# Kernel optimization log

Hardware: AMD Instinct MI355X
Metric: run time of the kernel (lower is better)

Reference implementation:

```python
import jax, jax.numpy as jnp
import numpy as np

LEVELS = 25  # constructor default, used in forward


def setup_inputs() -> dict:
    key = jax.random.key(0)
    ks = jax.random.split(key, 7)
    B, D_in, H, D_out = 131072, 512, 512, 128
    s_in = 1.0 / np.sqrt(D_in)
    s_h = 1.0 / np.sqrt(H)
    return {
        "x": jax.random.normal(ks[0], (B, D_in), jnp.float32),
        "W_in": jax.random.uniform(ks[1], (D_in, H), jnp.float32, -s_in, s_in),
        "b_in": jax.random.uniform(ks[2], (H,), jnp.float32, -s_in, s_in),
        "W_h": jax.random.uniform(ks[3], (H, H), jnp.float32, -s_h, s_h),
        "b_h": jax.random.uniform(ks[4], (H,), jnp.float32, -s_h, s_h),
        "W_out": jax.random.uniform(ks[5], (H, D_out), jnp.float32, -s_h, s_h),
        "b_out": jax.random.uniform(ks[6], (D_out,), jnp.float32, -s_h, s_h),
    }


def _discretize(x, levels):
    # Equal-width bins per column: np.linspace(min, max, levels+1)[1:-1]
    # -> levels-1 interior boundaries: min + (max-min)*k/levels, k=1..levels-1
    b_min = x.min(axis=0)  # [D]
    b_max = x.max(axis=0)  # [D]
    frac = jnp.arange(1, levels, dtype=x.dtype) / levels  # [levels-1]
    bounds = b_min[:, None] + (b_max - b_min)[:, None] * frac[None, :]  # [D, levels-1]
    # torch.bucketize(right=False) == searchsorted side='left', per column
    idx = jax.vmap(
        lambda col, b: jnp.searchsorted(b, col, side="left"),
        in_axes=(1, 0), out_axes=1,
    )(x, bounds)  # [B, D] int32
    # torch.tensor(X_discre, dtype=float32) detaches from the graph
    return jax.lax.stop_gradient(idx.astype(jnp.float32))


def reference(x, W_in, b_in, W_h, b_h, W_out, b_out):
    d = _discretize(x, LEVELS)                 # [B, D_in]
    h = jax.nn.relu(d @ W_in + b_in)           # l_in
    for _ in range(5):
        h = jax.nn.relu(h @ W_h + b_h)
    y = jax.nn.relu(h @ W_out + b_out)         # l_out
    d2_loss = jnp.zeros((), jnp.float32)
    return (y, d2_loss)
```

## Files before the change

### kernel.cpp

```cpp
#include <hip/hip_runtime.h>
#include <hip/hip_bf16.h>

typedef unsigned short u16;
typedef unsigned int u32;
typedef __attribute__((ext_vector_type(8))) short s16x8;
typedef __attribute__((ext_vector_type(4))) float f32x4;

__device__ __forceinline__ u16 bf16bits(float v) {
    union { __hip_bfloat16 b; u16 u; } c;
    c.b = __float2bfloat16(v);
    return c.u;
}

__device__ __forceinline__ float disc1(float v, float mn, float rg, float s) {
    const float u = __fmul_rn(__fsub_rn(v, mn), s);
    const float rn = rintf(u);
    int idx;
    if (fabsf(u - rn) > 1e-3f) {
        idx = (int)ceilf(u) - 1;
    } else {
        int kc = (int)rn;
        kc = kc < 1 ? 1 : (kc > 24 ? 24 : kc);
        const float cf = __fdiv_rn((float)kc, 25.0f);
        const float b = __fadd_rn(mn, __fmul_rn(rg, cf));
        idx = (int)rn - 1 + ((b < v) ? 1 : 0);
    }
    idx = idx < 0 ? 0 : (idx > 24 ? 24 : idx);
    return (float)idx;
}

__global__ void kminmax(const float* __restrict__ x, float* __restrict__ pmin,
                        float* __restrict__ pmax) {
    __shared__ float4 smn[512], smx[512];
    const int t = threadIdx.x;
    const int c4 = t & 127;
    const int ro = t >> 7;
    const size_t r0 = (size_t)blockIdx.x * 128;
    float4 mn = {1e30f, 1e30f, 1e30f, 1e30f};
    float4 mx = {-1e30f, -1e30f, -1e30f, -1e30f};
#pragma unroll 8
    for (int i = 0; i < 32; ++i) {
        const int row = ro + i * 4;
        const float4 v = ((const float4*)(x + (r0 + row) * 512))[c4];
        mn.x = fminf(mn.x, v.x); mn.y = fminf(mn.y, v.y);
        mn.z = fminf(mn.z, v.z); mn.w = fminf(mn.w, v.w);
        mx.x = fmaxf(mx.x, v.x); mx.y = fmaxf(mx.y, v.y);
        mx.z = fmaxf(mx.z, v.z); mx.w = fmaxf(mx.w, v.w);
    }
    smn[t] = mn; smx[t] = mx;
    __syncthreads();
    if (t < 128) {
#pragma unroll
        for (int p = 1; p < 4; ++p) {
            const float4 a = smn[t + p * 128], b = smx[t + p * 128];
            mn.x = fminf(mn.x, a.x); mn.y = fminf(mn.y, a.y);
            mn.z = fminf(mn.z, a.z); mn.w = fminf(mn.w, a.w);
            mx.x = fmaxf(mx.x, b.x); mx.y = fmaxf(mx.y, b.y);
            mx.z = fmaxf(mx.z, b.z); mx.w = fmaxf(mx.w, b.w);
        }
        ((float4*)(pmin + blockIdx.x * 512))[c4] = mn;
        ((float4*)(pmax + blockIdx.x * 512))[c4] = mx;
    }
}

__global__ void kred(const float* __restrict__ pmin, const float* __restrict__ pmax,
                     float* __restrict__ p2min, float* __restrict__ p2max, int per) {
    const int c = threadIdx.x;
    const int j = blockIdx.x;
    float mn = 1e30f, mx = -1e30f;
    for (int i = 0; i < per; ++i) {
        mn = fminf(mn, pmin[(size_t)(j * per + i) * 512 + c]);
        mx = fmaxf(mx, pmax[(size_t)(j * per + i) * 512 + c]);
    }
    p2min[j * 512 + c] = mn;
    p2max[j * 512 + c] = mx;
}

__global__ void kbounds(const float* __restrict__ p2min, const float* __restrict__ p2max,
                        float* __restrict__ cmin, float* __restrict__ crange,
                        float* __restrict__ sinv, int np, float* __restrict__ dloss) {
    const int c = threadIdx.x;
    float mn = 1e30f, mx = -1e30f;
    for (int p = 0; p < np; ++p) {
        mn = fminf(mn, p2min[p * 512 + c]);
        mx = fmaxf(mx, p2max[p * 512 + c]);
    }
    cmin[c] = mn;
    const float rg = __fsub_rn(mx, mn);
    crange[c] = rg;
    sinv[c] = __fdiv_rn(25.0f, rg);
    if (c == 0) dloss[0] = 0.0f;
}

__global__ void ktc_all(const float* __restrict__ W_in, const float* __restrict__ W_h,
                        const float* __restrict__ W_out,
                        __hip_bfloat16* __restrict__ WinT, __hip_bfloat16* __restrict__ WhT,
                        __hip_bfloat16* __restrict__ WoutT) {
    const int i = blockIdx.x * 256 + threadIdx.x;
    if (i < 512 * 512) {
        WinT[i] = __float2bfloat16(W_in[(size_t)(i & 511) * 512 + (i >> 9)]);
    } else if (i < 2 * 512 * 512) {
        const int j = i - 512 * 512;
        WhT[j] = __float2bfloat16(W_h[(size_t)(j & 511) * 512 + (j >> 9)]);
    } else if (i < 2 * 512 * 512 + 128 * 512) {
        const int j = i - 2 * 512 * 512;
        WoutT[j] = __float2bfloat16(W_out[(size_t)(j & 511) * 128 + (j >> 9)]);
    }
}

__global__ __launch_bounds__(512, 2) void megamlp(
    const float* __restrict__ x,
    const float* __restrict__ cmin, const float* __restrict__ crange,
    const float* __restrict__ sinv,
    const u16* __restrict__ WinT, const u16* __restrict__ WhT,
    const u16* __restrict__ WoutT,
    const float* __restrict__ b_in, const float* __restrict__ b_h,
    const float* __restrict__ b_out,
    float* __restrict__ out) {
    __shared__ __attribute__((aligned(16))) u16 actA[64 * 512];
    __shared__ __attribute__((aligned(16))) u16 actB[64 * 512];

    const int t = threadIdx.x;
    const int lane = t & 63;
    const int w = t >> 6;
    const int lr = lane & 15;
    const int kq = lane >> 4;
    const int xr = lr & 7;
    const size_t row0 = (size_t)blockIdx.x * 128;

    {
        const int c4 = t & 127;
        const int ro = t >> 7;
        const float4 mn4 = ((const float4*)cmin)[c4];
        const float4 rg4 = ((const float4*)crange)[c4];
        const float4 s4  = ((const float4*)sinv)[c4];
        const int g16 = c4 >> 1;
        const int hb  = (c4 & 1) << 3;
#pragma unroll 8
        for (int i = 0; i < 32; ++i) {
            const int row = ro + i * 4;
            const float4 v = ((const float4*)(x + (row0 + row) * 512))[c4];
            const u32 lo = (u32)bf16bits(disc1(v.x, mn4.x, rg4.x, s4.x))
                         | ((u32)bf16bits(disc1(v.y, mn4.y, rg4.y, s4.y)) << 16);
            const u32 hi = (u32)bf16bits(disc1(v.z, mn4.z, rg4.z, s4.z))
                         | ((u32)bf16bits(disc1(v.w, mn4.w, rg4.w, s4.w)) << 16);
            const int rl = row & 63;
            const int gg = g16 ^ (rl & 7);
            char* base = (row < 64) ? (char*)actA : (char*)actB;
            *(uint2*)(base + (rl << 10) + (gg << 4) + hb) = make_uint2(lo, hi);
        }
    }
    __syncthreads();

    for (int layer = 0; layer < 6; ++layer) {
        const u16* W = (layer == 0) ? WinT : WhT;
        const float* bias = (layer == 0) ? b_in : b_h;

        f32x4 acc[2][4][4] = {};
        const u16* wp0 = W + ((w * 64 + lr) << 9) + (kq << 3);

        s16x8 aF[4], aN[4];
#pragma unroll
        for (int mt = 0; mt < 4; ++mt)
            aF[mt] = *(const s16x8*)(wp0 + (mt << 13));

#pragma unroll
        for (int ks = 0; ks < 16; ++ks) {
            if (ks < 15) {
                const u16* wn = wp0 + (ks + 1) * 32;
#pragma unroll
                for (int mt = 0; mt < 4; ++mt)
                    aN[mt] = *(const s16x8*)(wn + (mt << 13));
            }
            const int gg = ((ks << 2) | kq) ^ xr;
#pragma unroll
            for (int h = 0; h < 2; ++h) {
                const char* ah = h ? (const char*)actB : (const char*)actA;
                s16x8 bF[4];
#pragma unroll
                for (int nt = 0; nt < 4; ++nt)
                    bF[nt] = *(const s16x8*)(ah + ((nt * 16 + lr) << 10) + (gg << 4));
#pragma unroll
                for (int mt = 0; mt < 4; ++mt)
#pragma unroll
                    for (int nt = 0; nt < 4; ++nt)
                        acc[h][mt][nt] = __builtin_amdgcn_mfma_f32_16x16x32_bf16(
                            aF[mt], bF[nt], acc[h][mt][nt], 0, 0, 0);
            }
#pragma unroll
            for (int mt = 0; mt < 4; ++mt) aF[mt] = aN[mt];
        }
        __syncthreads();

#pragma unroll
        for (int mt = 0; mt < 4; ++mt) {
            const int g16 = w * 8 + mt * 2 + (kq >> 1);
            float bv[4];
#pragma unroll
            for (int r = 0; r < 4; ++r)
                bv[r] = bias[w * 64 + mt * 16 + kq * 4 + r];
#pragma unroll
            for (int h = 0; h < 2; ++h) {
                char* ah = h ? (char*)actB : (char*)actA;
#pragma unroll
                for (int nt = 0; nt < 4; ++nt) {
                    const int batch = nt * 16 + lr;
                    const float v0 = fmaxf(acc[h][mt][nt][0] + bv[0], 0.0f);
                    const float v1 = fmaxf(acc[h][mt][nt][1] + bv[1], 0.0f);
                    const float v2 = fmaxf(acc[h][mt][nt][2] + bv[2], 0.0f);
                    const float v3 = fmaxf(acc[h][mt][nt][3] + bv[3], 0.0f);
                    const u32 lo = (u32)bf16bits(v0) | ((u32)bf16bits(v1) << 16);
                    const u32 hi = (u32)bf16bits(v2) | ((u32)bf16bits(v3) << 16);
                    const int gg = g16 ^ (batch & 7);
                    *(uint2*)(ah + (batch << 10) + (gg << 4) + ((kq & 1) << 3)) =
                        make_uint2(lo, hi);
                }
            }
        }
        __syncthreads();
    }

    {
        f32x4 acc[2][4] = {};
        const u16* wp = WoutT + ((w * 16 + lr) << 9) + (kq << 3);
        s16x8 aF = *(const s16x8*)(wp);
#pragma unroll
        for (int ks = 0; ks < 16; ++ks) {
            s16x8 aN;
            if (ks < 15) aN = *(const s16x8*)(wp + (ks + 1) * 32);
            const int gg = ((ks << 2) | kq) ^ xr;
#pragma unroll
            for (int h = 0; h < 2; ++h) {
                const char* ah = h ? (const char*)actB : (const char*)actA;
#pragma unroll
                for (int nt = 0; nt < 4; ++nt) {
                    const s16x8 bF = *(const s16x8*)(ah + ((nt * 16 + lr) << 10) + (gg << 4));
                    acc[h][nt] = __builtin_amdgcn_mfma_f32_16x16x32_bf16(
                        aF, bF, acc[h][nt], 0, 0, 0);
                }
            }
            aF = aN;
        }
        __syncthreads();

        float bv[4];
#pragma unroll
        for (int r = 0; r < 4; ++r) bv[r] = b_out[w * 16 + kq * 4 + r];
        const int g16o = w * 4 + kq;
#pragma unroll
        for (int h = 0; h < 2; ++h) {
            char* sh = h ? (char*)actB : (char*)actA;
#pragma unroll
            for (int nt = 0; nt < 4; ++nt) {
                const int batch = nt * 16 + lr;
                const int gg = g16o ^ (batch & 7);
                float* p = (float*)(sh + (batch << 9) + (gg << 4));
#pragma unroll
                for (int r = 0; r < 4; ++r)
                    p[r] = fmaxf(acc[h][nt][r] + bv[r], 0.0f);
            }
        }
    }
    __syncthreads();

    {
        const int n4 = t & 31;
        const int bo = t >> 5;
#pragma unroll
        for (int h = 0; h < 2; ++h) {
            const char* sh = h ? (const char*)actB : (const char*)actA;
#pragma unroll
            for (int pp = 0; pp < 4; ++pp) {
                const int batch = pp * 16 + bo;
                const int gg = n4 ^ (batch & 7);
                const float4 v = *(const float4*)(sh + (batch << 9) + (gg << 4));
                ((float4*)(out + (row0 + h * 64 + batch) * 128))[n4] = v;
            }
        }
    }
}

extern "C" void kernel_launch(void* const* d_in, const int* in_sizes, int n_in,
                              void* d_out, int out_size, void* d_ws, size_t ws_size,
                              hipStream_t stream) {
    const float* x     = (const float*)d_in[0];
    const float* W_in  = (const float*)d_in[1];
    const float* b_in  = (const float*)d_in[2];
    const float* W_h   = (const float*)d_in[3];
    const float* b_h   = (const float*)d_in[4];
    const float* W_out = (const float*)d_in[5];
    const float* b_out = (const float*)d_in[6];
    float* out = (float*)d_out;

    const int B = in_sizes[0] / 512;
    const int NP1 = B / 128;

    __hip_bfloat16* WinT  = (__hip_bfloat16*)d_ws;
    __hip_bfloat16* WhT   = WinT + 512 * 512;
    __hip_bfloat16* WoutT = WhT + 512 * 512;
    float* pmin   = (float*)(WoutT + 128 * 512);
    float* pmax   = pmin + (size_t)NP1 * 512;
    float* p2min  = pmax + (size_t)NP1 * 512;
    float* p2max  = p2min + 64 * 512;
    float* cmin   = p2max + 64 * 512;
    float* crange = cmin + 512;
    float* sinv   = crange + 512;

    kminmax<<<NP1, 512, 0, stream>>>(x, pmin, pmax);
    kred<<<64, 512, 0, stream>>>(pmin, pmax, p2min, p2max, NP1 / 64);
    kbounds<<<1, 512, 0, stream>>>(p2min, p2max, cmin, crange, sinv, 64,
                                   out + (size_t)B * 128);
    ktc_all<<<(2 * 512 * 512 + 128 * 512 + 255) / 256, 256, 0, stream>>>(
        W_in, W_h, W_out, WinT, WhT, WoutT);

    megamlp<<<B / 128, 512, 0, stream>>>(x, cmin, crange, sinv,
        (const u16*)WinT, (const u16*)WhT, (const u16*)WoutT,
        b_in, b_h, b_out, out);
}
```

Baseline: 956.0 us.

## Halve rows per block in fused MLP to raise occupancy

Each block of the fused MLP kernel now processes 64 batch rows instead of 128, using a single 64 KB LDS activation buffer instead of two. Launch bounds are raised to 4 blocks per CU and the grid doubles. The register prefetch of weight fragments for the next k-step is dropped, and bias loads become vectorized. The aim is more resident waves to hide latency, at the cost of reading each weight fragment from global/L2 twice as often per row processed.

```diff
diff --git a/kernel.cpp b/kernel.cpp
--- a/kernel.cpp
+++ b/kernel.cpp
@@ -108,7 +108,7 @@
     }
 }
 
-__global__ __launch_bounds__(512, 2) void megamlp(
+__global__ __launch_bounds__(512, 4) void megamlp(
     const float* __restrict__ x,
     const float* __restrict__ cmin, const float* __restrict__ crange,
     const float* __restrict__ sinv,
@@ -117,8 +117,7 @@
     const float* __restrict__ b_in, const float* __restrict__ b_h,
     const float* __restrict__ b_out,
     float* __restrict__ out) {
-    __shared__ __attribute__((aligned(16))) u16 actA[64 * 512];
-    __shared__ __attribute__((aligned(16))) u16 actB[64 * 512];
+    __shared__ __attribute__((aligned(16))) u16 act[64 * 512];
 
     const int t = threadIdx.x;
     const int lane = t & 63;
@@ -126,7 +125,7 @@
     const int lr = lane & 15;
     const int kq = lane >> 4;
     const int xr = lr & 7;
-    const size_t row0 = (size_t)blockIdx.x * 128;
+    const size_t row0 = (size_t)blockIdx.x * 64;
 
     {
         const int c4 = t & 127;
@@ -136,18 +135,16 @@
         const float4 s4  = ((const float4*)sinv)[c4];
         const int g16 = c4 >> 1;
         const int hb  = (c4 & 1) << 3;
-#pragma unroll 8
-        for (int i = 0; i < 32; ++i) {
+#pragma unroll 4
+        for (int i = 0; i < 16; ++i) {
             const int row = ro + i * 4;
             const float4 v = ((const float4*)(x + (row0 + row) * 512))[c4];
             const u32 lo = (u32)bf16bits(disc1(v.x, mn4.x, rg4.x, s4.x))
                          | ((u32)bf16bits(disc1(v.y, mn4.y, rg4.y, s4.y)) << 16);
             const u32 hi = (u32)bf16bits(disc1(v.z, mn4.z, rg4.z, s4.z))
                          | ((u32)bf16bits(disc1(v.w, mn4.w, rg4.w, s4.w)) << 16);
-            const int rl = row & 63;
-            const int gg = g16 ^ (rl & 7);
-            char* base = (row < 64) ? (char*)actA : (char*)actB;
-            *(uint2*)(base + (rl << 10) + (gg << 4) + hb) = make_uint2(lo, hi);
+            const int gg = g16 ^ (row & 7);
+            *(uint2*)((char*)act + (row << 10) + (gg << 4) + hb) = make_uint2(lo, hi);
         }
     }
     __syncthreads();
@@ -156,109 +153,76 @@
         const u16* W = (layer == 0) ? WinT : WhT;
         const float* bias = (layer == 0) ? b_in : b_h;
 
-        f32x4 acc[2][4][4] = {};
+        f32x4 acc[4][4] = {};
         const u16* wp0 = W + ((w * 64 + lr) << 9) + (kq << 3);
 
-        s16x8 aF[4], aN[4];
-#pragma unroll
-        for (int mt = 0; mt < 4; ++mt)
-            aF[mt] = *(const s16x8*)(wp0 + (mt << 13));
-
 #pragma unroll
         for (int ks = 0; ks < 16; ++ks) {
-            if (ks < 15) {
-                const u16* wn = wp0 + (ks + 1) * 32;
-#pragma unroll
-                for (int mt = 0; mt < 4; ++mt)
-                    aN[mt] = *(const s16x8*)(wn + (mt << 13));
-            }
+            s16x8 aF[4], bF[4];
+            const u16* wp = wp0 + ks * 32;
+#pragma unroll
+            for (int mt = 0; mt < 4; ++mt)
+                aF[mt] = *(const s16x8*)(wp + (mt << 13));
             const int gg = ((ks << 2) | kq) ^ xr;
 #pragma unroll
-            for (int h = 0; h < 2; ++h) {
-                const char* ah = h ? (const char*)actB : (const char*)actA;
-                s16x8 bF[4];
+            for (int nt = 0; nt < 4; ++nt)
+                bF[nt] = *(const s16x8*)((const char*)act + ((nt * 16 + lr) << 10) + (gg << 4));
+#pragma unroll
+            for (int mt = 0; mt < 4; ++mt)
 #pragma unroll
                 for (int nt = 0; nt < 4; ++nt)
-                    bF[nt] = *(const s16x8*)(ah + ((nt * 16 + lr) << 10) + (gg << 4));
-#pragma unroll
-                for (int mt = 0; mt < 4; ++mt)
-#pragma unroll
-                    for (int nt = 0; nt < 4; ++nt)
-                        acc[h][mt][nt] = __builtin_amdgcn_mfma_f32_16x16x32_bf16(
-                            aF[mt], bF[nt], acc[h][mt][nt], 0, 0, 0);
-            }
-#pragma unroll
-            for (int mt = 0; mt < 4; ++mt) aF[mt] = aN[mt];
+                    acc[mt][nt] = __builtin_amdgcn_mfma_f32_16x16x32_bf16(
+                        aF[mt], bF[nt], acc[mt][nt], 0, 0, 0);
         }
         __syncthreads();
 
 #pragma unroll
         for (int mt = 0; mt < 4; ++mt) {
+            const f32x4 bv = ((const f32x4*)bias)[w * 16 + mt * 4 + kq];
             const int g16 = w * 8 + mt * 2 + (kq >> 1);
-            float bv[4];
-#pragma unroll
-            for (int r = 0; r < 4; ++r)
-                bv[r] = bias[w * 64 + mt * 16 + kq * 4 + r];
-#pragma unroll
-            for (int h = 0; h < 2; ++h) {
-                char* ah = h ? (char*)actB : (char*)actA;
-#pragma unroll
-                for (int nt = 0; nt < 4; ++nt) {
-                    const int batch = nt * 16 + lr;
-                    const float v0 = fmaxf(acc[h][mt][nt][0] + bv[0], 0.0f);
-                    const float v1 = fmaxf(acc[h][mt][nt][1] + bv[1], 0.0f);
-                    const float v2 = fmaxf(acc[h][mt][nt][2] + bv[2], 0.0f);
-                    const float v3 = fmaxf(acc[h][mt][nt][3] + bv[3], 0.0f);
-                    const u32 lo = (u32)bf16bits(v0) | ((u32)bf16bits(v1) << 16);
-                    const u32 hi = (u32)bf16bits(v2) | ((u32)bf16bits(v3) << 16);
-                    const int gg = g16 ^ (batch & 7);
-                    *(uint2*)(ah + (batch << 10) + (gg << 4) + ((kq & 1) << 3)) =
-                        make_uint2(lo, hi);
-                }
-            }
-        }
-        __syncthreads();
-    }
-
-    {
-        f32x4 acc[2][4] = {};
-        const u16* wp = WoutT + ((w * 16 + lr) << 9) + (kq << 3);
-        s16x8 aF = *(const s16x8*)(wp);
-#pragma unroll
-        for (int ks = 0; ks < 16; ++ks) {
-            s16x8 aN;
-            if (ks < 15) aN = *(const s16x8*)(wp + (ks + 1) * 32);
-            const int gg = ((ks << 2) | kq) ^ xr;
-#pragma unroll
-            for (int h = 0; h < 2; ++h) {
-                const char* ah = h ? (const char*)actB : (const char*)actA;
-#pragma unroll
-                for (int nt = 0; nt < 4; ++nt) {
-                    const s16x8 bF = *(const s16x8*)(ah + ((nt * 16 + lr) << 10) + (gg << 4));
-                    acc[h][nt] = __builtin_amdgcn_mfma_f32_16x16x32_bf16(
-                        aF, bF, acc[h][nt], 0, 0, 0);
-                }
-            }
-            aF = aN;
-        }
-        __syncthreads();
-
-        float bv[4];
-#pragma unroll
-        for (int r = 0; r < 4; ++r) bv[r] = b_out[w * 16 + kq * 4 + r];
-        const int g16o = w * 4 + kq;
-#pragma unroll
-        for (int h = 0; h < 2; ++h) {
-            char* sh = h ? (char*)actB : (char*)actA;
 #pragma unroll
             for (int nt = 0; nt < 4; ++nt) {
                 const int batch = nt * 16 + lr;
-                const int gg = g16o ^ (batch & 7);
-                float* p = (float*)(sh + (batch << 9) + (gg << 4));
-#pragma unroll
-                for (int r = 0; r < 4; ++r)
-                    p[r] = fmaxf(acc[h][nt][r] + bv[r], 0.0f);
+                const float v0 = fmaxf(acc[mt][nt][0] + bv[0], 0.0f);
+                const float v1 = fmaxf(acc[mt][nt][1] + bv[1], 0.0f);
+                const float v2 = fmaxf(acc[mt][nt][2] + bv[2], 0.0f);
+                const float v3 = fmaxf(acc[mt][nt][3] + bv[3], 0.0f);
+                const u32 lo = (u32)bf16bits(v0) | ((u32)bf16bits(v1) << 16);
+                const u32 hi = (u32)bf16bits(v2) | ((u32)bf16bits(v3) << 16);
+                const int gg = g16 ^ (batch & 7);
+                *(uint2*)((char*)act + (batch << 10) + (gg << 4) + ((kq & 1) << 3)) =
+                    make_uint2(lo, hi);
             }
+        }
+        __syncthreads();
+    }
+
+    {
+        f32x4 acc[4] = {};
+        const u16* wp = WoutT + ((w * 16 + lr) << 9) + (kq << 3);
+#pragma unroll
+        for (int ks = 0; ks < 16; ++ks) {
+            const s16x8 aF = *(const s16x8*)(wp + ks * 32);
+            const int gg = ((ks << 2) | kq) ^ xr;
+#pragma unroll
+            for (int nt = 0; nt < 4; ++nt) {
+                const s16x8 bF = *(const s16x8*)((const char*)act + ((nt * 16 + lr) << 10) + (gg << 4));
+                acc[nt] = __builtin_amdgcn_mfma_f32_16x16x32_bf16(
+                    aF, bF, acc[nt], 0, 0, 0);
+            }
+        }
+        __syncthreads();
+
+        const f32x4 bvo = ((const f32x4*)b_out)[w * 4 + kq];
+        const int g16o = w * 4 + kq;
+#pragma unroll
+        for (int nt = 0; nt < 4; ++nt) {
+            const int batch = nt * 16 + lr;
+            const int gg = g16o ^ (batch & 7);
+            float* p = (float*)((char*)act + (batch << 9) + (gg << 4));
+#pragma unroll
+            for (int r = 0; r < 4; ++r)
+                p[r] = fmaxf(acc[nt][r] + bvo[r], 0.0f);
         }
     }
     __syncthreads();
@@ -267,15 +231,11 @@
         const int n4 = t & 31;
         const int bo = t >> 5;
 #pragma unroll
-        for (int h = 0; h < 2; ++h) {
-            const char* sh = h ? (const char*)actB : (const char*)actA;
-#pragma unroll
-            for (int pp = 0; pp < 4; ++pp) {
-                const int batch = pp * 16 + bo;
-                const int gg = n4 ^ (batch & 7);
-                const float4 v = *(const float4*)(sh + (batch << 9) + (gg << 4));
-                ((float4*)(out + (row0 + h * 64 + batch) * 128))[n4] = v;
-            }
+        for (int pp = 0; pp < 4; ++pp) {
+            const int batch = pp * 16 + bo;
+            const int gg = n4 ^ (batch & 7);
+            const float4 v = *(const float4*)((const char*)act + (batch << 9) + (gg << 4));
+            ((float4*)(out + (row0 + batch) * 128))[n4] = v;
         }
     }
 }
@@ -313,7 +273,7 @@
     ktc_all<<<(2 * 512 * 512 + 128 * 512 + 255) / 256, 256, 0, stream>>>(
         W_in, W_h, W_out, WinT, WhT, WoutT);
 
-    megamlp<<<B / 128, 512, 0, stream>>>(x, cmin, crange, sinv,
+    megamlp<<<B / 64, 512, 0, stream>>>(x, cmin, crange, sinv,
         (const u16*)WinT, (const u16*)WhT, (const u16*)WoutT,
         b_in, b_h, b_out, out);
 }
```

Result: slower. 1.200 ms (+25.5%).

## Switch hidden layers to 32x32x16 MFMA tiles with setprio around MFMA bursts

Applied to the files above, without the earlier changes.

Replaces the 16x16x32 bf16 MFMA tiling in the six 512x512 layers with 32x32x16 MFMAs on 2x2 tiles per half-batch. This cuts the number of LDS fragment loads per MFMA and the instruction count. It also drops the explicit register double-buffering of weight fragments, wraps MFMA bursts in s_setprio, and vectorizes the bias loads. The cost is the epilogue remapping to the 32x32 accumulator layout and possibly more exposed global-load latency on the weight fragments.

```diff
diff --git a/kernel.cpp b/kernel.cpp
--- a/kernel.cpp
+++ b/kernel.cpp
@@ -5,6 +5,7 @@
 typedef unsigned int u32;
 typedef __attribute__((ext_vector_type(8))) short s16x8;
 typedef __attribute__((ext_vector_type(4))) float f32x4;
+typedef __attribute__((ext_vector_type(16))) float f32x16;
 
 __device__ __forceinline__ u16 bf16bits(float v) {
     union { __hip_bfloat16 b; u16 u; } c;
@@ -126,6 +127,8 @@
     const int lr = lane & 15;
     const int kq = lane >> 4;
     const int xr = lr & 7;
+    const int l31 = lane & 31;
+    const int lh = lane >> 5;
     const size_t row0 = (size_t)blockIdx.x * 128;
 
     {
@@ -156,64 +159,58 @@
         const u16* W = (layer == 0) ? WinT : WhT;
         const float* bias = (layer == 0) ? b_in : b_h;
 
-        f32x4 acc[2][4][4] = {};
-        const u16* wp0 = W + ((w * 64 + lr) << 9) + (kq << 3);
-
-        s16x8 aF[4], aN[4];
-#pragma unroll
-        for (int mt = 0; mt < 4; ++mt)
-            aF[mt] = *(const s16x8*)(wp0 + (mt << 13));
-
-#pragma unroll
-        for (int ks = 0; ks < 16; ++ks) {
-            if (ks < 15) {
-                const u16* wn = wp0 + (ks + 1) * 32;
-#pragma unroll
-                for (int mt = 0; mt < 4; ++mt)
-                    aN[mt] = *(const s16x8*)(wn + (mt << 13));
-            }
-            const int gg = ((ks << 2) | kq) ^ xr;
+        f32x16 acc[2][2][2] = {};
+        const u16* wpA = W + ((w * 64 + l31) << 9) + (lh << 3);
+
+#pragma unroll
+        for (int ks = 0; ks < 32; ++ks) {
+            s16x8 aF[2], bF[2][2];
+#pragma unroll
+            for (int mt = 0; mt < 2; ++mt)
+                aF[mt] = *(const s16x8*)(wpA + (mt << 14) + (ks << 4));
+            const int gg = ((ks << 1) | lh) ^ (l31 & 7);
 #pragma unroll
             for (int h = 0; h < 2; ++h) {
                 const char* ah = h ? (const char*)actB : (const char*)actA;
-                s16x8 bF[4];
-#pragma unroll
-                for (int nt = 0; nt < 4; ++nt)
-                    bF[nt] = *(const s16x8*)(ah + ((nt * 16 + lr) << 10) + (gg << 4));
-#pragma unroll
-                for (int mt = 0; mt < 4; ++mt)
-#pragma unroll
-                    for (int nt = 0; nt < 4; ++nt)
-                        acc[h][mt][nt] = __builtin_amdgcn_mfma_f32_16x16x32_bf16(
-                            aF[mt], bF[nt], acc[h][mt][nt], 0, 0, 0);
-            }
-#pragma unroll
-            for (int mt = 0; mt < 4; ++mt) aF[mt] = aN[mt];
+#pragma unroll
+                for (int nt = 0; nt < 2; ++nt)
+                    bF[h][nt] = *(const s16x8*)(ah + ((nt * 32 + l31) << 10) + (gg << 4));
+            }
+            __builtin_amdgcn_s_setprio(1);
+#pragma unroll
+            for (int h = 0; h < 2; ++h)
+#pragma unroll
+                for (int mt = 0; mt < 2; ++mt)
+#pragma unroll
+                    for (int nt = 0; nt < 2; ++nt)
+                        acc[h][mt][nt] = __builtin_amdgcn_mfma_f32_32x32x16_bf16(
+                            aF[mt], bF[h][nt], acc[h][mt][nt], 0, 0, 0);
+            __builtin_amdgcn_s_setprio(0);
         }
         __syncthreads();
 
 #pragma unroll
-        for (int mt = 0; mt < 4; ++mt) {
-            const int g16 = w * 8 + mt * 2 + (kq >> 1);
-            float bv[4];
-#pragma unroll
-            for (int r = 0; r < 4; ++r)
-                bv[r] = bias[w * 64 + mt * 16 + kq * 4 + r];
-#pragma unroll
-            for (int h = 0; h < 2; ++h) {
-                char* ah = h ? (char*)actB : (char*)actA;
-#pragma unroll
-                for (int nt = 0; nt < 4; ++nt) {
-                    const int batch = nt * 16 + lr;
-                    const float v0 = fmaxf(acc[h][mt][nt][0] + bv[0], 0.0f);
-                    const float v1 = fmaxf(acc[h][mt][nt][1] + bv[1], 0.0f);
-                    const float v2 = fmaxf(acc[h][mt][nt][2] + bv[2], 0.0f);
-                    const float v3 = fmaxf(acc[h][mt][nt][3] + bv[3], 0.0f);
-                    const u32 lo = (u32)bf16bits(v0) | ((u32)bf16bits(v1) << 16);
-                    const u32 hi = (u32)bf16bits(v2) | ((u32)bf16bits(v3) << 16);
-                    const int gg = g16 ^ (batch & 7);
-                    *(uint2*)(ah + (batch << 10) + (gg << 4) + ((kq & 1) << 3)) =
-                        make_uint2(lo, hi);
+        for (int mt = 0; mt < 2; ++mt) {
+#pragma unroll
+            for (int q = 0; q < 4; ++q) {
+                const f32x4 bv = ((const f32x4*)bias)[w * 16 + mt * 8 + q * 2 + lh];
+                const int g16 = w * 8 + mt * 4 + q;
+#pragma unroll
+                for (int h = 0; h < 2; ++h) {
+                    char* ah = h ? (char*)actB : (char*)actA;
+#pragma unroll
+                    for (int nt = 0; nt < 2; ++nt) {
+                        const int rl = nt * 32 + l31;
+                        const float v0 = fmaxf(acc[h][mt][nt][q * 4 + 0] + bv[0], 0.0f);
+                        const float v1 = fmaxf(acc[h][mt][nt][q * 4 + 1] + bv[1], 0.0f);
+                        const float v2 = fmaxf(acc[h][mt][nt][q * 4 + 2] + bv[2], 0.0f);
+                        const float v3 = fmaxf(acc[h][mt][nt][q * 4 + 3] + bv[3], 0.0f);
+                        const u32 lo = (u32)bf16bits(v0) | ((u32)bf16bits(v1) << 16);
+                        const u32 hi = (u32)bf16bits(v2) | ((u32)bf16bits(v3) << 16);
+                        const int gg = g16 ^ (rl & 7);
+                        *(uint2*)(ah + (rl << 10) + (gg << 4) + (lh << 3)) =
+                            make_uint2(lo, hi);
+                    }
                 }
             }
         }
@@ -223,12 +220,11 @@
     {
         f32x4 acc[2][4] = {};
         const u16* wp = WoutT + ((w * 16 + lr) << 9) + (kq << 3);
-        s16x8 aF = *(const s16x8*)(wp);
 #pragma unroll
         for (int ks = 0; ks < 16; ++ks) {
-            s16x8 aN;
-            if (ks < 15) aN = *(const s16x8*)(wp + (ks + 1) * 32);
+            const s16x8 aF = *(const s16x8*)(wp + ks * 32);
             const int gg = ((ks << 2) | kq) ^ xr;
+            __builtin_amdgcn_s_setprio(1);
 #pragma unroll
             for (int h = 0; h < 2; ++h) {
                 const char* ah = h ? (const char*)actB : (const char*)actA;
@@ -239,13 +235,11 @@
                         aF, bF, acc[h][nt], 0, 0, 0);
                 }
             }
-            aF = aN;
+            __builtin_amdgcn_s_setprio(0);
         }
         __syncthreads();
 
-        float bv[4];
-#pragma unroll
-        for (int r = 0; r < 4; ++r) bv[r] = b_out[w * 16 + kq * 4 + r];
+        const f32x4 bvo = ((const f32x4*)b_out)[w * 4 + kq];
         const int g16o = w * 4 + kq;
 #pragma unroll
         for (int h = 0; h < 2; ++h) {
@@ -257,7 +251,7 @@
                 float* p = (float*)(sh + (batch << 9) + (gg << 4));
 #pragma unroll
                 for (int r = 0; r < 4; ++r)
-                    p[r] = fmaxf(acc[h][nt][r] + bv[r], 0.0f);
+                    p[r] = fmaxf(acc[h][nt][r] + bvo[r], 0.0f);
             }
         }
     }
```

New measurement: 932.0 us. 2.5% less time.
